# Kernel tuning notes

Hardware: AMD Instinct MI355X
Metric: run time of the kernel (lower is better)

Reference implementation:

```python
import jax, jax.numpy as jnp
import numpy as np

N_NODES, N_EDGES, CH, FEAT = 20000, 320000, 256, 118


def setup_inputs() -> dict:
    key = jax.random.key(0)
    ks = jax.random.split(key, 8)
    x = jax.random.uniform(ks[0], (N_NODES, FEAT), dtype=jnp.float32)
    edge_index = jax.random.randint(ks[1], (2, N_EDGES), 0, N_NODES, dtype=jnp.int64)
    s = 0.05
    W_embed = jax.random.normal(ks[2], (FEAT, CH), dtype=jnp.float32) * s
    b_embed = jnp.zeros((CH,), jnp.float32)
    W1 = jax.random.normal(ks[3], (CH, CH), dtype=jnp.float32) * s
    b1 = jnp.zeros((CH,), jnp.float32)
    W2 = jax.random.normal(ks[4], (CH, CH), dtype=jnp.float32) * s
    b2 = jnp.zeros((CH,), jnp.float32)
    return {"x": x, "edge_index": edge_index, "W_embed": W_embed, "b_embed": b_embed,
            "W1": W1, "b1": b1, "W2": W2, "b2": b2}


def reference(x, edge_index, W_embed, b_embed, W1, b1, W2, b2):
    n = x.shape[0]
    # node embedding: Linear(118 -> C)
    h = x @ W_embed + b_embed  # [N, C]
    src, dst = edge_index[0], edge_index[1]
    # message: gather x_j per edge, dense1 + exact GELU (dropout = identity in eval)
    msg = jax.nn.gelu(h[src] @ W1 + b1, approximate=False)  # [E, C]
    # mean aggregation into destination nodes
    agg = jax.ops.segment_sum(msg, dst, num_segments=n)  # [N, C]
    cnt = jax.ops.segment_sum(jnp.ones((msg.shape[0],), msg.dtype), dst, num_segments=n)
    agg = agg / jnp.maximum(cnt, 1.0)[:, None]
    # update: dense2 + exact GELU
    out = jax.nn.gelu(agg @ W2 + b2, approximate=False)  # [N, C]
    # final mean over channel dim
    return out.mean(axis=1)  # [N]
```

## Files before the change

kernel.cpp:

```cpp
#include <hip/hip_runtime.h>
#include <math.h>

#define N_NODES 20000
#define N_EDGES 320000
#define CH      256
#define FEAT    118
#define CAP     48

typedef float    f32x4 __attribute__((ext_vector_type(4)));
typedef short    s16x8 __attribute__((ext_vector_type(8)));
typedef _Float16 f16x4 __attribute__((ext_vector_type(4)));
typedef _Float16 f16x8 __attribute__((ext_vector_type(8)));
typedef unsigned short u16;

union Frag  { s16x8 v; u16 u[8]; };
union FragH { f16x8 v; _Float16 h[8]; };

__device__ __forceinline__ float gelu_exact(float x) {
    return 0.5f * x * (1.0f + erff(x * 0.70710678118654752f));
}
__device__ __forceinline__ u16 f2bf(float f) {
    unsigned u = __float_as_uint(f);
    u = (u + 0x7FFFu + ((u >> 16) & 1u)) >> 16;
    return (u16)u;
}
__device__ __forceinline__ float bf2f(u16 h) { return __uint_as_float(((unsigned)h) << 16); }

__global__ __launch_bounds__(256) void prep0(const float* __restrict__ We,
                                             const float* __restrict__ be,
                                             const float* __restrict__ W1,
                                             const float* __restrict__ b1,
                                             const float* __restrict__ W2,
                                             _Float16* __restrict__ w2h, _Float16* __restrict__ w2l,
                                             u16* __restrict__ wch, u16* __restrict__ wcl,
                                             float* __restrict__ bc,
                                             int* __restrict__ cnt) {
    const int b = blockIdx.x, tid = threadIdx.x;
    if (b < 32) {
        int fid = b * 256 + tid;
        int lane = fid & 63, ks = (fid >> 6) & 7, nt = fid >> 9;
        int n = nt * 16 + (lane & 15);
        int k0 = ks * 32 + (lane >> 4) * 8;
        FragH hi, lo;
        #pragma unroll
        for (int j = 0; j < 8; j++) {
            float v = W2[(size_t)(k0 + j) * 256 + n];
            _Float16 h = (_Float16)v;
            hi.h[j] = h;
            lo.h[j] = (_Float16)((v - (float)h) * 4096.0f);
        }
        ((f16x8*)w2h)[fid] = hi.v;
        ((f16x8*)w2l)[fid] = lo.v;
    } else if (b < 161) {
        int f = b - 32;
        int n = tid;
        if (f < 128) {
            float acc = 0.0f;
            if (f < FEAT) {
                const float* wr = We + (size_t)f * 256;
                #pragma unroll 8
                for (int c = 0; c < 256; c++) acc += wr[c] * W1[(size_t)c * 256 + n];
            }
            int nt = n >> 4, lm = n & 15, ks = f >> 5, q = (f >> 3) & 3, j = f & 7;
            size_t idx = (((size_t)nt * 4 + ks) * 64 + q * 16 + lm) * 8 + j;
            u16 h = f2bf(acc);
            wch[idx] = h;
            wcl[idx] = f2bf(acc - bf2f(h));
        } else {
            float acc = b1[n];
            #pragma unroll 8
            for (int c = 0; c < 256; c++) acc += be[c] * W1[(size_t)c * 256 + n];
            bc[n] = acc;
        }
    } else {
        int idx = (b - 161) * 256 + tid;
        if (idx < N_NODES) cnt[idx] = 0;
    }
}

__global__ __launch_bounds__(256) void main_fused(const float* __restrict__ x,
                                                  const int* __restrict__ ei,
                                                  const u16* __restrict__ Bh_, const u16* __restrict__ Bl_,
                                                  const float* __restrict__ bias,
                                                  int* __restrict__ cnt, int* __restrict__ bins,
                                                  _Float16* __restrict__ Mout) {
    if (blockIdx.x >= 1250) {
        int e = (blockIdx.x - 1250) * 256 + threadIdx.x;
        int s = ei[e];
        int d = ei[N_EDGES + e];
        int p = atomicAdd(&cnt[d], 1);
        if (p < CAP) bins[(size_t)d * CAP + p] = s;
        return;
    }
    __shared__ float xs[16][132];
    __shared__ _Float16 Ls[16][256];
    const int tid = threadIdx.x, wave = tid >> 6, lane = tid & 63;
    const int quad = lane >> 4, lm = lane & 15;
    const int mt = blockIdx.x, nt0 = wave * 4;
    {
        int r = tid >> 4, ci = tid & 15;
        const float* xrow = x + (size_t)(mt * 16 + r) * FEAT;
        #pragma unroll
        for (int it = 0; it < 8; it++) {
            int col = ci + it * 16;
            xs[r][col] = (col < FEAT) ? xrow[col] : 0.0f;
        }
    }
    __syncthreads();
    s16x8 a_h[4], a_l[4];
    #pragma unroll
    for (int ks = 0; ks < 4; ks++) {
        int k0 = ks * 32 + quad * 8;
        Frag hi, lo;
        #pragma unroll
        for (int j = 0; j < 8; j++) {
            float v = xs[lm][k0 + j];
            u16 h = f2bf(v);
            hi.u[j] = h; lo.u[j] = f2bf(v - bf2f(h));
        }
        a_h[ks] = hi.v; a_l[ks] = lo.v;
    }
    const s16x8* Bh = (const s16x8*)Bh_; const s16x8* Bl = (const s16x8*)Bl_;
    f32x4 acc[4] = {f32x4{0,0,0,0}, f32x4{0,0,0,0}, f32x4{0,0,0,0}, f32x4{0,0,0,0}};
    #pragma unroll
    for (int ks = 0; ks < 4; ks++) {
        #pragma unroll
        for (int t = 0; t < 4; t++) {
            s16x8 bh = Bh[((size_t)(nt0 + t) * 4 + ks) * 64 + lane];
            s16x8 bl = Bl[((size_t)(nt0 + t) * 4 + ks) * 64 + lane];
            acc[t] = __builtin_amdgcn_mfma_f32_16x16x32_bf16(a_h[ks], bh, acc[t], 0, 0, 0);
            acc[t] = __builtin_amdgcn_mfma_f32_16x16x32_bf16(a_l[ks], bh, acc[t], 0, 0, 0);
            acc[t] = __builtin_amdgcn_mfma_f32_16x16x32_bf16(a_h[ks], bl, acc[t], 0, 0, 0);
        }
    }
    #pragma unroll
    for (int t = 0; t < 4; t++) {
        float bn = bias[(nt0 + t) * 16 + lm];
        #pragma unroll
        for (int r = 0; r < 4; r++)
            Ls[quad * 4 + r][(nt0 + t) * 16 + lm] = (_Float16)gelu_exact(acc[t][r] + bn);
    }
    __syncthreads();
    s16x8* dst = (s16x8*)Mout + (size_t)mt * 512;
    const s16x8* src = (const s16x8*)&Ls[0][0];
    dst[tid]       = src[tid];
    dst[256 + tid] = src[256 + tid];
}

__global__ __launch_bounds__(256) void aggregate(const _Float16* __restrict__ M,
                                                 const int* __restrict__ cnt,
                                                 const int* __restrict__ bins,
                                                 _Float16* __restrict__ aggf) {
    int node = (blockIdx.x * 256 + threadIdx.x) >> 6;
    int lane = threadIdx.x & 63;
    int half = lane >> 5, lh = lane & 31;
    int c = cnt[node];
    int cc = min(c, CAP);
    int myid = (lane < cc) ? bins[(size_t)node * CAP + lane] : 0;
    float a[8] = {0.f, 0.f, 0.f, 0.f, 0.f, 0.f, 0.f, 0.f};
    for (int j = 0; j < cc; j += 16) {
        f16x8 v[8];
        #pragma unroll
        for (int u = 0; u < 8; u++) {
            int e = min(j + u * 2 + half, cc - 1);
            int s = __shfl(myid, e, 64);
            v[u] = *(const f16x8*)(M + (size_t)s * CH + lh * 8);
        }
        #pragma unroll
        for (int u = 0; u < 8; u++) {
            if (j + u * 2 + half < cc) {
                #pragma unroll
                for (int q = 0; q < 8; q++) a[q] += (float)v[u][q];
            }
        }
    }
    #pragma unroll
    for (int q = 0; q < 8; q++) a[q] += __shfl_xor(a[q], 32, 64);
    if (half == 0) {
        float inv = 1.0f / (float)max(c, 1);
        FragH o;
        #pragma unroll
        for (int q = 0; q < 8; q++) o.h[q] = (_Float16)(a[q] * inv);
        int mt = node >> 4, lm = node & 15;
        int ks = lh >> 2, quad = lh & 3;
        size_t base = (((size_t)mt * 8 + ks) * 64 + quad * 16 + lm) * 8;
        *(f16x8*)(aggf + base) = o.v;
    }
}

__global__ __launch_bounds__(256) void gemm_mean(const _Float16* __restrict__ Af_,
                                                 const _Float16* __restrict__ Bh_, const _Float16* __restrict__ Bl_,
                                                 const float* __restrict__ bias,
                                                 float* __restrict__ out) {
    __shared__ float part[4][32];
    const int tid = threadIdx.x, wave = tid >> 6, lane = tid & 63;
    const int quad = lane >> 4, lm = lane & 15;
    const int mt0 = blockIdx.x * 2, nt0 = wave * 4;
    const f16x8* Af = (const f16x8*)Af_;
    const f16x8* Bh = (const f16x8*)Bh_; const f16x8* Bl = (const f16x8*)Bl_;
    f32x4 acch[2][4], accl[2][4];
    #pragma unroll
    for (int mi = 0; mi < 2; mi++)
        #pragma unroll
        for (int t = 0; t < 4; t++) {
            acch[mi][t] = f32x4{0.f, 0.f, 0.f, 0.f};
            accl[mi][t] = f32x4{0.f, 0.f, 0.f, 0.f};
        }
    #pragma unroll
    for (int ks = 0; ks < 8; ks++) {
        f16x8 a0 = Af[((size_t)(mt0 + 0) * 8 + ks) * 64 + lane];
        f16x8 a1 = Af[((size_t)(mt0 + 1) * 8 + ks) * 64 + lane];
        #pragma unroll
        for (int t = 0; t < 4; t++) {
            f16x8 bh = Bh[((size_t)(nt0 + t) * 8 + ks) * 64 + lane];
            f16x8 bl = Bl[((size_t)(nt0 + t) * 8 + ks) * 64 + lane];
            acch[0][t] = __builtin_amdgcn_mfma_f32_16x16x32_f16(a0, bh, acch[0][t], 0, 0, 0);
            accl[0][t] = __builtin_amdgcn_mfma_f32_16x16x32_f16(a0, bl, accl[0][t], 0, 0, 0);
            acch[1][t] = __builtin_amdgcn_mfma_f32_16x16x32_f16(a1, bh, acch[1][t], 0, 0, 0);
            accl[1][t] = __builtin_amdgcn_mfma_f32_16x16x32_f16(a1, bl, accl[1][t], 0, 0, 0);
        }
    }
    float p[2][4] = {{0.f,0.f,0.f,0.f},{0.f,0.f,0.f,0.f}};
    #pragma unroll
    for (int t = 0; t < 4; t++) {
        float bn = bias[(nt0 + t) * 16 + lm];
        #pragma unroll
        for (int mi = 0; mi < 2; mi++)
            #pragma unroll
            for (int r = 0; r < 4; r++)
                p[mi][r] += gelu_exact(acch[mi][t][r] + accl[mi][t][r] * (1.0f / 4096.0f) + bn);
    }
    #pragma unroll
    for (int off = 1; off < 16; off <<= 1)
        #pragma unroll
        for (int mi = 0; mi < 2; mi++)
            #pragma unroll
            for (int r = 0; r < 4; r++)
                p[mi][r] += __shfl_xor(p[mi][r], off, 64);
    if (lm == 0)
        #pragma unroll
        for (int mi = 0; mi < 2; mi++)
            #pragma unroll
            for (int r = 0; r < 4; r++)
                part[wave][mi * 16 + quad * 4 + r] = p[mi][r];
    __syncthreads();
    if (tid < 32) {
        float s = part[0][tid] + part[1][tid] + part[2][tid] + part[3][tid];
        out[blockIdx.x * 32 + tid] = s * (1.0f / 256.0f);
    }
}

extern "C" void kernel_launch(void* const* d_in, const int* in_sizes, int n_in,
                              void* d_out, int out_size, void* d_ws, size_t ws_size,
                              hipStream_t stream) {
    const float* x  = (const float*)d_in[0];
    const int*   ei = (const int*)d_in[1];
    const float* We = (const float*)d_in[2];
    const float* be = (const float*)d_in[3];
    const float* W1 = (const float*)d_in[4];
    const float* b1 = (const float*)d_in[5];
    const float* W2 = (const float*)d_in[6];
    const float* b2 = (const float*)d_in[7];
    float* out = (float*)d_out;

    char* ws = (char*)d_ws;
    size_t off = 0;
    _Float16* M = (_Float16*)(ws + off); off += 10240000;
    _Float16* aggf = (_Float16*)(ws + off); off += 10240000;
    u16* wch = (u16*)(ws + off); off += 65536;
    u16* wcl = (u16*)(ws + off); off += 65536;
    _Float16* w2h = (_Float16*)(ws + off); off += 131072;
    _Float16* w2l = (_Float16*)(ws + off); off += 131072;
    float* bc = (float*)(ws + off); off += 1024;
    int* cnt  = (int*)(ws + off); off += N_NODES * 4;
    int* bins = (int*)(ws + off); off += (size_t)N_NODES * CAP * 4;

    prep0<<<240, 256, 0, stream>>>(We, be, W1, b1, W2, w2h, w2l, wch, wcl, bc, cnt);
    main_fused<<<2500, 256, 0, stream>>>(x, ei, wch, wcl, bc, cnt, bins, M);
    aggregate<<<N_NODES / 4, 256, 0, stream>>>(M, cnt, bins, aggf);
    gemm_mean<<<N_NODES / 32, 256, 0, stream>>>(aggf, w2h, w2l, b2, out);
}
```

Before: 150.5 us.

## Split aggregation across channel slices with 16 nodes per wave

Rewrites the aggregate kernel so each block handles a 32-channel slice (one of 8) for 64 nodes, with each wave covering 16 nodes and 4 lanes per node. Every lane loads its neighbour ids directly from the bins array instead of broadcasting them by shuffle, and the cross-half reduction is removed. The aim is more independent gathers in flight per wave and better locality of the M slices across blocks. In exchange, each node's bin list is re-read by all 8 slice blocks, each gather moves only 64 contiguous bytes, and waves can diverge when neighbour counts differ.

Measured after the change: 157.1 us. 4.3% more time.

```diff
diff --git a/kernel.cpp b/kernel.cpp
--- a/kernel.cpp
+++ b/kernel.cpp
@@ -151,39 +151,42 @@
                                                  const int* __restrict__ cnt,
                                                  const int* __restrict__ bins,
                                                  _Float16* __restrict__ aggf) {
-    int node = (blockIdx.x * 256 + threadIdx.x) >> 6;
-    int lane = threadIdx.x & 63;
-    int half = lane >> 5, lh = lane & 31;
-    int c = cnt[node];
+    const int sl = blockIdx.x & 7;
+    const int grp = blockIdx.x >> 3;
+    const int tid = threadIdx.x;
+    const int wave = tid >> 6, lane = tid & 63;
+    const int nsub = lane >> 2, q4 = lane & 3;
+    const int node = grp * 64 + wave * 16 + nsub;
+    const bool valid = node < N_NODES;
+    int c  = valid ? cnt[node] : 0;
     int cc = min(c, CAP);
-    int myid = (lane < cc) ? bins[(size_t)node * CAP + lane] : 0;
+    const size_t binb = (size_t)node * CAP;
+    const _Float16* Msl = M + sl * 32 + q4 * 8;
     float a[8] = {0.f, 0.f, 0.f, 0.f, 0.f, 0.f, 0.f, 0.f};
-    for (int j = 0; j < cc; j += 16) {
+    for (int j = 0; j < cc; j += 8) {
+        int ids[8];
+        #pragma unroll
+        for (int u = 0; u < 8; u++)
+            ids[u] = bins[binb + min(j + u, cc - 1)];
         f16x8 v[8];
         #pragma unroll
+        for (int u = 0; u < 8; u++)
+            v[u] = *(const f16x8*)(Msl + (size_t)ids[u] * CH);
+        #pragma unroll
         for (int u = 0; u < 8; u++) {
-            int e = min(j + u * 2 + half, cc - 1);
-            int s = __shfl(myid, e, 64);
-            v[u] = *(const f16x8*)(M + (size_t)s * CH + lh * 8);
-        }
-        #pragma unroll
-        for (int u = 0; u < 8; u++) {
-            if (j + u * 2 + half < cc) {
+            if (j + u < cc) {
                 #pragma unroll
                 for (int q = 0; q < 8; q++) a[q] += (float)v[u][q];
             }
         }
     }
-    #pragma unroll
-    for (int q = 0; q < 8; q++) a[q] += __shfl_xor(a[q], 32, 64);
-    if (half == 0) {
+    if (valid) {
         float inv = 1.0f / (float)max(c, 1);
         FragH o;
         #pragma unroll
         for (int q = 0; q < 8; q++) o.h[q] = (_Float16)(a[q] * inv);
         int mt = node >> 4, lm = node & 15;
-        int ks = lh >> 2, quad = lh & 3;
-        size_t base = (((size_t)mt * 8 + ks) * 64 + quad * 16 + lm) * 8;
+        size_t base = (((size_t)mt * 8 + sl) * 64 + q4 * 16 + lm) * 8;
         *(f16x8*)(aggf + base) = o.v;
     }
 }
@@ -277,6 +280,6 @@
 
     prep0<<<240, 256, 0, stream>>>(We, be, W1, b1, W2, w2h, w2l, wch, wcl, bc, cnt);
     main_fused<<<2500, 256, 0, stream>>>(x, ei, wch, wcl, bc, cnt, bins, M);
-    aggregate<<<N_NODES / 4, 256, 0, stream>>>(M, cnt, bins, aggf);
+    aggregate<<<313 * 8, 256, 0, stream>>>(M, cnt, bins, aggf);
     gemm_mean<<<N_NODES / 32, 256, 0, stream>>>(aggf, w2h, w2l, b2, out);
 }
```
